# Optimization experiments

Hardware: AMD Instinct MI355X
Metric: run time of the kernel (lower is better)

The kernel has to match this reference:

```python
import jax, jax.numpy as jnp
import numpy as np

B, N, K, C, CE, H = 2, 2048, 48, 128, 128, 128
IN = 2 * C + CE  # 384
AGG_SCALE = 30.0
LN_EPS = 1e-5


def setup_inputs() -> dict:
    key = jax.random.key(0)
    ks = jax.random.split(key, 12)
    inp = {
        "node_h": jax.random.normal(ks[0], (B, N, C), jnp.float32),
        "edge_h": jax.random.normal(ks[1], (B, N, K, CE), jnp.float32),
        "edge_index": jax.random.randint(ks[2], (B, N, K), 0, N, jnp.int64),
        # message MLP: Linear(IN,H) GELU Linear(H,H) GELU Linear(H,C)
        "W1": jax.random.normal(ks[3], (IN, H), jnp.float32) / np.sqrt(IN),
        "b1": jnp.zeros((H,), jnp.float32),
        "W2": jax.random.normal(ks[4], (H, H), jnp.float32) / np.sqrt(H),
        "b2": jnp.zeros((H,), jnp.float32),
        "W3": jax.random.normal(ks[5], (H, C), jnp.float32) / np.sqrt(H),
        "b3": jnp.zeros((C,), jnp.float32),
        "Wu": jax.random.normal(ks[6], (C, C), jnp.float32) / np.sqrt(C),
        "bu": jnp.zeros((C,), jnp.float32),
        "ln_g": jnp.ones((C,), jnp.float32),
        "ln_b": jnp.zeros((C,), jnp.float32),
    }
    return inp


def _layer_norm(x, g, b):
    mu = jnp.mean(x, axis=-1, keepdims=True)
    var = jnp.var(x, axis=-1, keepdims=True)
    return (x - mu) * jax.lax.rsqrt(var + LN_EPS) * g + b


def _gelu(x):
    return jax.nn.gelu(x, approximate=False)  # torch nn.GELU default (erf)


def reference(node_h, edge_h, edge_index, W1, b1, W2, b2, W3, b3, Wu, bu, ln_g, ln_b):
    b, n, k = edge_index.shape
    c = node_h.shape[-1]
    # gather neighbor node features: (B,N,K,C)
    node_j = jnp.take_along_axis(
        node_h, edge_index.reshape(b, n * k)[..., None], axis=1
    ).reshape(b, n, k, c)
    node_i = jnp.broadcast_to(node_h[:, :, None, :], (b, n, k, c))
    edge_packed = jnp.concatenate([node_i, node_j, edge_h], axis=-1)  # (B,N,K,IN)
    # message MLP
    h = _gelu(edge_packed @ W1 + b1)
    h = _gelu(h @ W2 + b2)
    messages = (h @ W3 + b3).sum(axis=-2) / AGG_SCALE  # (B,N,C)
    # dropout is identity in eval mode
    updated_nodes = _layer_norm(node_h + messages, ln_g, ln_b)
    node_updates = updated_nodes @ Wu + bu
    out = _layer_norm(node_h + node_updates, ln_g, ln_b)
    return out
```

## Files before the change

kernel.cpp:

```cpp
#include <hip/hip_runtime.h>
#include <hip/hip_bf16.h>
#include <math.h>

#define Bn   2
#define Nn   2048
#define Kn   48
#define Cn   128
#define G2   16

typedef short bf16x8 __attribute__((ext_vector_type(8)));
typedef float f32x4  __attribute__((ext_vector_type(4)));

#if __has_builtin(__builtin_amdgcn_cvt_pk_bf16_f32)
#define HAS_PK 1
#endif

__device__ __forceinline__ short f2bf(float f) {
  union { float f; unsigned u; } v; v.f = f;
  unsigned r = v.u + 0x7fffu + ((v.u >> 16) & 1u);
  return (short)(r >> 16);
}

__device__ __forceinline__ unsigned pk2(float a, float b) {
#ifdef HAS_PK
  auto p = __builtin_amdgcn_cvt_pk_bf16_f32(a, b);
  return __builtin_bit_cast(unsigned, p);
#else
  return (unsigned)(unsigned short)f2bf(a) | ((unsigned)(unsigned short)f2bf(b) << 16);
#endif
}

__device__ __forceinline__ float gelu_f(float x) {
  float z = x * (-2.3021991f - 0.10294200f * x * x);
  float e = __builtin_amdgcn_exp2f(z);
  return x * __builtin_amdgcn_rcpf(1.0f + e);
}

__global__ void pack_weights(const float* __restrict__ W1,
                             const float* __restrict__ W2,
                             const float* __restrict__ W3,
                             const float* __restrict__ Wu,
                             short* __restrict__ ws) {
  int tid = blockIdx.x * blockDim.x + threadIdx.x;
  if (tid >= 192 * 64) return;
  int lane = tid & 63;
  int tile = tid >> 6;
  const float* W; short* dst;
  if (tile < 32)       { W = W1;         dst = ws; }
  else if (tile < 96)  { W = W1 + 16384; dst = ws + 16384; tile -= 32; }
  else if (tile < 128) { W = W2;         dst = ws + 49152; tile -= 96; }
  else if (tile < 160) { W = W3;         dst = ws + 65536; tile -= 128; }
  else                 { W = Wu;         dst = ws + 81920; tile -= 160; }
  int kt = tile >> 3, nt = tile & 7;
  int n  = nt * 16 + (lane & 15);
  int k0 = kt * 32 + (lane >> 4) * 8;
  union { short s[8]; bf16x8 v; } u8;
#pragma unroll
  for (int j = 0; j < 8; j++) u8.s[j] = f2bf(W[(k0 + j) * 128 + n]);
  *reinterpret_cast<bf16x8*>(dst + (tile << 9) + lane * 8) = u8.v;
}

__global__ __launch_bounds__(512, 6)
void node_update_kernel(const float* __restrict__ node_h,
                        const float* __restrict__ edge_h,
                        const int*   __restrict__ edge_index,
                        const short* __restrict__ wpack,
                        const float* __restrict__ b1,
                        const float* __restrict__ b2,
                        float* __restrict__ hs_out) {
  __shared__ __align__(16) char smem[50048];
  short* Xs    = (short*)smem;
  short* H1s   = (short*)(smem + 24576);
  short* nhb   = (short*)(smem + 49152);
  int*   idx_s = (int*)  (smem + 49664);

  const int tid  = threadIdx.x;
  const int n0   = blockIdx.x * 2;
  const int bb   = n0 >> 11;
  const int lane = tid & 63;
  const int wave = tid >> 6;
  const int lr   = lane & 15;
  const int lq   = lane >> 4;

  const short* W1i = wpack;
  const short* W1e = wpack + 16384;
  const short* W2p = wpack + 49152;

  if (tid < 256) {
    nhb[tid] = f2bf(node_h[(size_t)n0 * Cn + tid]);
  } else if (tid < 352) {
    idx_s[tid - 256] = edge_index[n0 * Kn + (tid - 256)];
  }
  __syncthreads();

  {
    const int w  = tid & 31;
    const int rr = tid >> 5;
#pragma unroll
    for (int k = 0; k < 6; k++) {
      int r = rr + k * 16;
      const float* src = (w < 16)
          ? node_h + (size_t)(bb * Nn + idx_s[r]) * Cn + w * 8
          : edge_h + ((size_t)n0 * Kn + r) * Cn + (w - 16) * 8;
      float4 v0 = *reinterpret_cast<const float4*>(src);
      float4 v1 = *reinterpret_cast<const float4*>(src + 4);
      uint4 p;
      p.x = pk2(v0.x, v0.y); p.y = pk2(v0.z, v0.w);
      p.z = pk2(v1.x, v1.y); p.w = pk2(v1.z, v1.w);
      *reinterpret_cast<uint4*>(&Xs[r * 256 + ((w ^ (r & 7)) << 3)]) = p;
    }
  }

  f32x4 accY[2] = {};
#pragma unroll
  for (int kt = 0; kt < 4; kt++) {
    bf16x8 avA = {}, avB = {};
    if (lr == 0) {
      avA = *reinterpret_cast<const bf16x8*>(&nhb[kt * 32 + lq * 8]);
      avB = *reinterpret_cast<const bf16x8*>(&nhb[128 + kt * 32 + lq * 8]);
    }
    bf16x8 bv = *reinterpret_cast<const bf16x8*>(W1i + ((kt * 8 + wave) << 9) + lane * 8);
    accY[0] = __builtin_amdgcn_mfma_f32_16x16x32_bf16(avA, bv, accY[0], 0, 0, 0);
    accY[1] = __builtin_amdgcn_mfma_f32_16x16x32_bf16(avB, bv, accY[1], 0, 0, 0);
  }
  __syncthreads();

  f32x4 acc[6] = {};
#pragma unroll
  for (int kt = 0; kt < 8; kt++) {
    bf16x8 bf = *reinterpret_cast<const bf16x8*>(W1e + ((kt * 8 + wave) << 9) + lane * 8);
    int sw = (((kt * 4 + lq) ^ (lr & 7)) << 3);
#pragma unroll
    for (int m = 0; m < 6; m++) {
      bf16x8 a = *reinterpret_cast<const bf16x8*>(&Xs[(m * 16 + lr) * 256 + sw]);
      acc[m] = __builtin_amdgcn_mfma_f32_16x16x32_bf16(a, bf, acc[m], 0, 0, 0);
    }
  }
  __syncthreads();

  {
    int col = wave * 16 + lr;
    float yiA = __shfl(accY[0][0], lr) + b1[col];
    float yiB = __shfl(accY[1][0], lr) + b1[col];
    int g = col >> 3, cl = col & 7;
#pragma unroll
    for (int mt = 0; mt < 6; mt++) {
      float yi = (mt < 3) ? yiA : yiB;
      int r0 = mt * 16 + lq * 4;
      float g0 = gelu_f(acc[mt][0] + yi);
      float g1 = gelu_f(acc[mt][1] + yi);
      float g2 = gelu_f(acc[mt][2] + yi);
      float g3 = gelu_f(acc[mt][3] + yi);
      unsigned p01 = pk2(g0, g1), p23 = pk2(g2, g3);
      H1s[(r0 + 0) * 128 + ((g ^ ((r0 + 0) & 7)) << 3) + cl] = (short)(p01 & 0xffff);
      H1s[(r0 + 1) * 128 + ((g ^ ((r0 + 1) & 7)) << 3) + cl] = (short)(p01 >> 16);
      H1s[(r0 + 2) * 128 + ((g ^ ((r0 + 2) & 7)) << 3) + cl] = (short)(p23 & 0xffff);
      H1s[(r0 + 3) * 128 + ((g ^ ((r0 + 3) & 7)) << 3) + cl] = (short)(p23 >> 16);
    }
  }
  __syncthreads();

  f32x4 acc2[6] = {};
#pragma unroll
  for (int kt = 0; kt < 4; kt++) {
    bf16x8 bf = *reinterpret_cast<const bf16x8*>(W2p + ((kt * 8 + wave) << 9) + lane * 8);
    int sw = (((kt * 4 + lq) ^ (lr & 7)) << 3);
#pragma unroll
    for (int m = 0; m < 6; m++) {
      bf16x8 a = *reinterpret_cast<const bf16x8*>(&H1s[(m * 16 + lr) * 128 + sw]);
      acc2[m] = __builtin_amdgcn_mfma_f32_16x16x32_bf16(a, bf, acc2[m], 0, 0, 0);
    }
  }
  {
    int col = wave * 16 + lr;
    float bias = b2[col];
    float sA = 0.f, sB = 0.f;
#pragma unroll
    for (int mt = 0; mt < 3; mt++)
#pragma unroll
      for (int r = 0; r < 4; r++) {
        sA += gelu_f(acc2[mt][r] + bias);
        sB += gelu_f(acc2[mt + 3][r] + bias);
      }
    sA += __shfl_xor(sA, 16);
    sA += __shfl_xor(sA, 32);
    sB += __shfl_xor(sB, 16);
    sB += __shfl_xor(sB, 32);
    if (lq == 0) {
      hs_out[(size_t)n0 * Cn + col]       = sA;
      hs_out[(size_t)(n0 + 1) * Cn + col] = sB;
    }
  }
}

__global__ __launch_bounds__(256, 4)
void tail_kernel(const float* __restrict__ node_h,
                 const short* __restrict__ wpack,
                 const float* __restrict__ b3,
                 const float* __restrict__ bu,
                 const float* __restrict__ ln_g,
                 const float* __restrict__ ln_b,
                 float* __restrict__ out) {
  __shared__ __align__(16) char sm2[24832];
  short* hsB = (short*)sm2;
  float* nhr = (float*)(sm2 + 4096);
  float* xs  = (float*)(sm2 + 12288);
  short* usB = (short*)(sm2 + 20736);

  const int tid  = threadIdx.x;
  const int lane = tid & 63;
  const int wave = tid >> 6;
  const int lr   = lane & 15;
  const int lq   = lane >> 4;
  const int n0   = blockIdx.x * G2;

  const short* W3p = wpack + 65536;
  const short* Wup = wpack + 81920;

  {
    int row = tid >> 4, seg = tid & 15;
    const float* p = node_h + (size_t)(n0 + row) * Cn + seg * 8;
    float4 a0 = *reinterpret_cast<const float4*>(p);
    float4 a1 = *reinterpret_cast<const float4*>(p + 4);
    *reinterpret_cast<float4*>(&nhr[row * 128 + seg * 8])     = a0;
    *reinterpret_cast<float4*>(&nhr[row * 128 + seg * 8 + 4]) = a1;
    const float* q = out + (size_t)(n0 + row) * Cn + seg * 8;
    float4 c0 = *reinterpret_cast<const float4*>(q);
    float4 c1 = *reinterpret_cast<const float4*>(q + 4);
    uint4 pk;
    pk.x = pk2(c0.x, c0.y); pk.y = pk2(c0.z, c0.w);
    pk.z = pk2(c1.x, c1.y); pk.w = pk2(c1.z, c1.w);
    *reinterpret_cast<uint4*>(&hsB[row * 128 + ((seg ^ (row & 7)) << 3)]) = pk;
  }
  __syncthreads();

  f32x4 am[2] = {};
#pragma unroll
  for (int kt = 0; kt < 4; kt++) {
    bf16x8 av = *reinterpret_cast<const bf16x8*>(&hsB[lr * 128 + (((kt * 4 + lq) ^ (lr & 7)) << 3)]);
    bf16x8 bv0 = *reinterpret_cast<const bf16x8*>(W3p + ((kt * 8 + wave * 2 + 0) << 9) + lane * 8);
    bf16x8 bv1 = *reinterpret_cast<const bf16x8*>(W3p + ((kt * 8 + wave * 2 + 1) << 9) + lane * 8);
    am[0] = __builtin_amdgcn_mfma_f32_16x16x32_bf16(av, bv0, am[0], 0, 0, 0);
    am[1] = __builtin_amdgcn_mfma_f32_16x16x32_bf16(av, bv1, am[1], 0, 0, 0);
  }
#pragma unroll
  for (int j = 0; j < 2; j++) {
    int col = (wave * 2 + j) * 16 + lr;
    float bb = 48.0f * b3[col];
#pragma unroll
    for (int r = 0; r < 4; r++) {
      int row = lq * 4 + r;
      xs[row * 132 + col] = nhr[row * 128 + col] + (am[j][r] + bb) * (1.0f / 30.0f);
    }
  }
  __syncthreads();

  const float lg1 = ln_g[lane],      lb1v = ln_b[lane];
  const float lg2 = ln_g[lane + 64], lb2v = ln_b[lane + 64];
#pragma unroll
  for (int s = 0; s < 4; s++) {
    int row = wave * 4 + s;
    float v1 = xs[row * 132 + lane];
    float v2 = xs[row * 132 + lane + 64];
    float s1 = v1 + v2, s2 = v1 * v1 + v2 * v2;
#pragma unroll
    for (int off = 32; off >= 1; off >>= 1) {
      s1 += __shfl_xor(s1, off);
      s2 += __shfl_xor(s2, off);
    }
    float mu = s1 * (1.f / 128.f);
    float var = s2 * (1.f / 128.f) - mu * mu;
    float rstd = rsqrtf(var + 1e-5f);
    unsigned u12 = pk2((v1 - mu) * rstd * lg1 + lb1v,
                       (v2 - mu) * rstd * lg2 + lb2v);
    int sw = (row & 7);
    usB[row * 128 + (((lane >> 3) ^ sw) << 3) + (lane & 7)]       = (short)(u12 & 0xffff);
    usB[row * 128 + ((((lane >> 3) + 8) ^ sw) << 3) + (lane & 7)] = (short)(u12 >> 16);
  }
  __syncthreads();

  f32x4 au[2] = {};
#pragma unroll
  for (int kt = 0; kt < 4; kt++) {
    bf16x8 av = *reinterpret_cast<const bf16x8*>(&usB[lr * 128 + (((kt * 4 + lq) ^ (lr & 7)) << 3)]);
    bf16x8 bv0 = *reinterpret_cast<const bf16x8*>(Wup + ((kt * 8 + wave * 2 + 0) << 9) + lane * 8);
    bf16x8 bv1 = *reinterpret_cast<const bf16x8*>(Wup + ((kt * 8 + wave * 2 + 1) << 9) + lane * 8);
    au[0] = __builtin_amdgcn_mfma_f32_16x16x32_bf16(av, bv0, au[0], 0, 0, 0);
    au[1] = __builtin_amdgcn_mfma_f32_16x16x32_bf16(av, bv1, au[1], 0, 0, 0);
  }
  __syncthreads();
#pragma unroll
  for (int j = 0; j < 2; j++) {
    int col = (wave * 2 + j) * 16 + lr;
    float bb = bu[col];
#pragma unroll
    for (int r = 0; r < 4; r++) {
      int row = lq * 4 + r;
      xs[row * 132 + col] = nhr[row * 128 + col] + au[j][r] + bb;
    }
  }
  __syncthreads();

#pragma unroll
  for (int s = 0; s < 4; s++) {
    int row = wave * 4 + s;
    float v1 = xs[row * 132 + lane];
    float v2 = xs[row * 132 + lane + 64];
    float s1 = v1 + v2, s2 = v1 * v1 + v2 * v2;
#pragma unroll
    for (int off = 32; off >= 1; off >>= 1) {
      s1 += __shfl_xor(s1, off);
      s2 += __shfl_xor(s2, off);
    }
    float mu = s1 * (1.f / 128.f);
    float var = s2 * (1.f / 128.f) - mu * mu;
    float rstd = rsqrtf(var + 1e-5f);
    out[(size_t)(n0 + row) * Cn + lane]      = (v1 - mu) * rstd * lg1 + lb1v;
    out[(size_t)(n0 + row) * Cn + lane + 64] = (v2 - mu) * rstd * lg2 + lb2v;
  }
}

extern "C" void kernel_launch(void* const* d_in, const int* in_sizes, int n_in,
                              void* d_out, int out_size, void* d_ws, size_t ws_size,
                              hipStream_t stream) {
  const float* node_h     = (const float*)d_in[0];
  const float* edge_h     = (const float*)d_in[1];
  const int*   edge_index = (const int*)  d_in[2];
  const float* W1 = (const float*)d_in[3];
  const float* b1 = (const float*)d_in[4];
  const float* W2 = (const float*)d_in[5];
  const float* b2 = (const float*)d_in[6];
  const float* W3 = (const float*)d_in[7];
  const float* b3 = (const float*)d_in[8];
  const float* Wu = (const float*)d_in[9];
  const float* bu = (const float*)d_in[10];
  const float* ln_g = (const float*)d_in[11];
  const float* ln_b = (const float*)d_in[12];
  float* out   = (float*)d_out;
  short* wpack = (short*)d_ws;

  pack_weights<<<48, 256, 0, stream>>>(W1, W2, W3, Wu, wpack);
  node_update_kernel<<<(Bn * Nn) / 2, 512, 0, stream>>>(
      node_h, edge_h, edge_index, wpack, b1, b2, out);
  tail_kernel<<<(Bn * Nn) / G2, 256, 0, stream>>>(
      node_h, wpack, b3, bu, ln_g, ln_b, out);
}
```

Baseline: 206.7 us.

## Prefetch weights into registers and overlap gather loads with node-projection MFMA

After: 282.2 us. 1.37x slower.

```diff
diff --git a/kernel.cpp b/kernel.cpp
--- a/kernel.cpp
+++ b/kernel.cpp
@@ -86,6 +86,20 @@
   const short* W1e = wpack + 16384;
   const short* W2p = wpack + 49152;
 
+  bf16x8 w1i[4], w1e[8], w2f[4];
+#pragma unroll
+  for (int kt = 0; kt < 4; kt++)
+    w1i[kt] = *reinterpret_cast<const bf16x8*>(W1i + ((kt * 8 + wave) << 9) + lane * 8);
+#pragma unroll
+  for (int kt = 0; kt < 8; kt++)
+    w1e[kt] = *reinterpret_cast<const bf16x8*>(W1e + ((kt * 8 + wave) << 9) + lane * 8);
+#pragma unroll
+  for (int kt = 0; kt < 4; kt++)
+    w2f[kt] = *reinterpret_cast<const bf16x8*>(W2p + ((kt * 8 + wave) << 9) + lane * 8);
+  const int colw = wave * 16 + lr;
+  const float b1v = b1[colw];
+  const float b2v = b2[colw];
+
   if (tid < 256) {
     nhb[tid] = f2bf(node_h[(size_t)n0 * Cn + tid]);
   } else if (tid < 352) {
@@ -93,25 +107,21 @@
   }
   __syncthreads();
 
-  {
-    const int w  = tid & 31;
-    const int rr = tid >> 5;
-#pragma unroll
-    for (int k = 0; k < 6; k++) {
-      int r = rr + k * 16;
-      const float* src = (w < 16)
-          ? node_h + (size_t)(bb * Nn + idx_s[r]) * Cn + w * 8
-          : edge_h + ((size_t)n0 * Kn + r) * Cn + (w - 16) * 8;
-      float4 v0 = *reinterpret_cast<const float4*>(src);
-      float4 v1 = *reinterpret_cast<const float4*>(src + 4);
-      uint4 p;
-      p.x = pk2(v0.x, v0.y); p.y = pk2(v0.z, v0.w);
-      p.z = pk2(v1.x, v1.y); p.w = pk2(v1.z, v1.w);
-      *reinterpret_cast<uint4*>(&Xs[r * 256 + ((w ^ (r & 7)) << 3)]) = p;
-    }
+  const int w  = tid & 31;
+  const int rr = tid >> 5;
+  float4 v0[6], v1[6];
+#pragma unroll
+  for (int k = 0; k < 6; k++) {
+    int r = rr + k * 16;
+    const float* src = (w < 16)
+        ? node_h + (size_t)(bb * Nn + idx_s[r]) * Cn + w * 8
+        : edge_h + ((size_t)n0 * Kn + r) * Cn + (w - 16) * 8;
+    v0[k] = *reinterpret_cast<const float4*>(src);
+    v1[k] = *reinterpret_cast<const float4*>(src + 4);
   }
 
   f32x4 accY[2] = {};
+  __builtin_amdgcn_s_setprio(1);
 #pragma unroll
   for (int kt = 0; kt < 4; kt++) {
     bf16x8 avA = {}, avB = {};
@@ -119,30 +129,39 @@
       avA = *reinterpret_cast<const bf16x8*>(&nhb[kt * 32 + lq * 8]);
       avB = *reinterpret_cast<const bf16x8*>(&nhb[128 + kt * 32 + lq * 8]);
     }
-    bf16x8 bv = *reinterpret_cast<const bf16x8*>(W1i + ((kt * 8 + wave) << 9) + lane * 8);
-    accY[0] = __builtin_amdgcn_mfma_f32_16x16x32_bf16(avA, bv, accY[0], 0, 0, 0);
-    accY[1] = __builtin_amdgcn_mfma_f32_16x16x32_bf16(avB, bv, accY[1], 0, 0, 0);
+    accY[0] = __builtin_amdgcn_mfma_f32_16x16x32_bf16(avA, w1i[kt], accY[0], 0, 0, 0);
+    accY[1] = __builtin_amdgcn_mfma_f32_16x16x32_bf16(avB, w1i[kt], accY[1], 0, 0, 0);
+  }
+  __builtin_amdgcn_s_setprio(0);
+
+#pragma unroll
+  for (int k = 0; k < 6; k++) {
+    int r = rr + k * 16;
+    uint4 p;
+    p.x = pk2(v0[k].x, v0[k].y); p.y = pk2(v0[k].z, v0[k].w);
+    p.z = pk2(v1[k].x, v1[k].y); p.w = pk2(v1[k].z, v1[k].w);
+    *reinterpret_cast<uint4*>(&Xs[r * 256 + ((w ^ (r & 7)) << 3)]) = p;
   }
   __syncthreads();
 
   f32x4 acc[6] = {};
+  __builtin_amdgcn_s_setprio(1);
 #pragma unroll
   for (int kt = 0; kt < 8; kt++) {
-    bf16x8 bf = *reinterpret_cast<const bf16x8*>(W1e + ((kt * 8 + wave) << 9) + lane * 8);
     int sw = (((kt * 4 + lq) ^ (lr & 7)) << 3);
 #pragma unroll
     for (int m = 0; m < 6; m++) {
       bf16x8 a = *reinterpret_cast<const bf16x8*>(&Xs[(m * 16 + lr) * 256 + sw]);
-      acc[m] = __builtin_amdgcn_mfma_f32_16x16x32_bf16(a, bf, acc[m], 0, 0, 0);
-    }
-  }
+      acc[m] = __builtin_amdgcn_mfma_f32_16x16x32_bf16(a, w1e[kt], acc[m], 0, 0, 0);
+    }
+  }
+  __builtin_amdgcn_s_setprio(0);
   __syncthreads();
 
   {
-    int col = wave * 16 + lr;
-    float yiA = __shfl(accY[0][0], lr) + b1[col];
-    float yiB = __shfl(accY[1][0], lr) + b1[col];
-    int g = col >> 3, cl = col & 7;
+    float yiA = __shfl(accY[0][0], lr) + b1v;
+    float yiB = __shfl(accY[1][0], lr) + b1v;
+    int g = colw >> 3, cl = colw & 7;
 #pragma unroll
     for (int mt = 0; mt < 6; mt++) {
       float yi = (mt < 3) ? yiA : yiB;
@@ -161,34 +180,33 @@
   __syncthreads();
 
   f32x4 acc2[6] = {};
-#pragma unroll
-  for (int kt = 0; kt < 4; kt++) {
-    bf16x8 bf = *reinterpret_cast<const bf16x8*>(W2p + ((kt * 8 + wave) << 9) + lane * 8);
+  __builtin_amdgcn_s_setprio(1);
+#pragma unroll
+  for (int kt = 0; kt < 4; kt++) {
     int sw = (((kt * 4 + lq) ^ (lr & 7)) << 3);
 #pragma unroll
     for (int m = 0; m < 6; m++) {
       bf16x8 a = *reinterpret_cast<const bf16x8*>(&H1s[(m * 16 + lr) * 128 + sw]);
-      acc2[m] = __builtin_amdgcn_mfma_f32_16x16x32_bf16(a, bf, acc2[m], 0, 0, 0);
-    }
-  }
+      acc2[m] = __builtin_amdgcn_mfma_f32_16x16x32_bf16(a, w2f[kt], acc2[m], 0, 0, 0);
+    }
+  }
+  __builtin_amdgcn_s_setprio(0);
   {
-    int col = wave * 16 + lr;
-    float bias = b2[col];
     float sA = 0.f, sB = 0.f;
 #pragma unroll
     for (int mt = 0; mt < 3; mt++)
 #pragma unroll
       for (int r = 0; r < 4; r++) {
-        sA += gelu_f(acc2[mt][r] + bias);
-        sB += gelu_f(acc2[mt + 3][r] + bias);
+        sA += gelu_f(acc2[mt][r] + b2v);
+        sB += gelu_f(acc2[mt + 3][r] + b2v);
       }
     sA += __shfl_xor(sA, 16);
     sA += __shfl_xor(sA, 32);
     sB += __shfl_xor(sB, 16);
     sB += __shfl_xor(sB, 32);
     if (lq == 0) {
-      hs_out[(size_t)n0 * Cn + col]       = sA;
-      hs_out[(size_t)(n0 + 1) * Cn + col] = sB;
+      hs_out[(size_t)n0 * Cn + colw]       = sA;
+      hs_out[(size_t)(n0 + 1) * Cn + colw] = sB;
     }
   }
 }
@@ -216,6 +234,15 @@
 
   const short* W3p = wpack + 65536;
   const short* Wup = wpack + 81920;
+
+  bf16x8 w3f[8], wuf[8];
+#pragma unroll
+  for (int kt = 0; kt < 4; kt++) {
+    w3f[2 * kt + 0] = *reinterpret_cast<const bf16x8*>(W3p + ((kt * 8 + wave * 2 + 0) << 9) + lane * 8);
+    w3f[2 * kt + 1] = *reinterpret_cast<const bf16x8*>(W3p + ((kt * 8 + wave * 2 + 1) << 9) + lane * 8);
+    wuf[2 * kt + 0] = *reinterpret_cast<const bf16x8*>(Wup + ((kt * 8 + wave * 2 + 0) << 9) + lane * 8);
+    wuf[2 * kt + 1] = *reinterpret_cast<const bf16x8*>(Wup + ((kt * 8 + wave * 2 + 1) << 9) + lane * 8);
+  }
 
   {
     int row = tid >> 4, seg = tid & 15;
@@ -238,10 +265,8 @@
 #pragma unroll
   for (int kt = 0; kt < 4; kt++) {
     bf16x8 av = *reinterpret_cast<const bf16x8*>(&hsB[lr * 128 + (((kt * 4 + lq) ^ (lr & 7)) << 3)]);
-    bf16x8 bv0 = *reinterpret_cast<const bf16x8*>(W3p + ((kt * 8 + wave * 2 + 0) << 9) + lane * 8);
-    bf16x8 bv1 = *reinterpret_cast<const bf16x8*>(W3p + ((kt * 8 + wave * 2 + 1) << 9) + lane * 8);
-    am[0] = __builtin_amdgcn_mfma_f32_16x16x32_bf16(av, bv0, am[0], 0, 0, 0);
-    am[1] = __builtin_amdgcn_mfma_f32_16x16x32_bf16(av, bv1, am[1], 0, 0, 0);
+    am[0] = __builtin_amdgcn_mfma_f32_16x16x32_bf16(av, w3f[2 * kt + 0], am[0], 0, 0, 0);
+    am[1] = __builtin_amdgcn_mfma_f32_16x16x32_bf16(av, w3f[2 * kt + 1], am[1], 0, 0, 0);
   }
 #pragma unroll
   for (int j = 0; j < 2; j++) {
@@ -283,10 +308,8 @@
 #pragma unroll
   for (int kt = 0; kt < 4; kt++) {
     bf16x8 av = *reinterpret_cast<const bf16x8*>(&usB[lr * 128 + (((kt * 4 + lq) ^ (lr & 7)) << 3)]);
-    bf16x8 bv0 = *reinterpret_cast<const bf16x8*>(Wup + ((kt * 8 + wave * 2 + 0) << 9) + lane * 8);
-    bf16x8 bv1 = *reinterpret_cast<const bf16x8*>(Wup + ((kt * 8 + wave * 2 + 1) << 9) + lane * 8);
-    au[0] = __builtin_amdgcn_mfma_f32_16x16x32_bf16(av, bv0, au[0], 0, 0, 0);
-    au[1] = __builtin_amdgcn_mfma_f32_16x16x32_bf16(av, bv1, au[1], 0, 0, 0);
+    au[0] = __builtin_amdgcn_mfma_f32_16x16x32_bf16(av, wuf[2 * kt + 0], au[0], 0, 0, 0);
+    au[1] = __builtin_amdgcn_mfma_f32_16x16x32_bf16(av, wuf[2 * kt + 1], au[1], 0, 0, 0);
   }
   __syncthreads();
 #pragma unroll
```

## Split X staging into two K-halves to halve shared memory and raise occupancy

Applied to the files above, without the earlier changes.

Result: no change. 209.0 us (+1.1%).

```diff
diff --git a/kernel.cpp b/kernel.cpp
--- a/kernel.cpp
+++ b/kernel.cpp
@@ -60,7 +60,7 @@
   *reinterpret_cast<bf16x8*>(dst + (tile << 9) + lane * 8) = u8.v;
 }
 
-__global__ __launch_bounds__(512, 6)
+__global__ __launch_bounds__(512, 8)
 void node_update_kernel(const float* __restrict__ node_h,
                         const float* __restrict__ edge_h,
                         const int*   __restrict__ edge_index,
@@ -68,11 +68,11 @@
                         const float* __restrict__ b1,
                         const float* __restrict__ b2,
                         float* __restrict__ hs_out) {
-  __shared__ __align__(16) char smem[50048];
+  __shared__ __align__(16) char smem[25472];
   short* Xs    = (short*)smem;
-  short* H1s   = (short*)(smem + 24576);
-  short* nhb   = (short*)(smem + 49152);
-  int*   idx_s = (int*)  (smem + 49664);
+  short* H1s   = (short*)smem;
+  short* nhb   = (short*)(smem + 24576);
+  int*   idx_s = (int*)  (smem + 25088);
 
   const int tid  = threadIdx.x;
   const int n0   = blockIdx.x * 2;
@@ -93,23 +93,20 @@
   }
   __syncthreads();
 
-  {
-    const int w  = tid & 31;
-    const int rr = tid >> 5;
-#pragma unroll
-    for (int k = 0; k < 6; k++) {
-      int r = rr + k * 16;
-      const float* src = (w < 16)
-          ? node_h + (size_t)(bb * Nn + idx_s[r]) * Cn + w * 8
-          : edge_h + ((size_t)n0 * Kn + r) * Cn + (w - 16) * 8;
-      float4 v0 = *reinterpret_cast<const float4*>(src);
-      float4 v1 = *reinterpret_cast<const float4*>(src + 4);
-      uint4 p;
-      p.x = pk2(v0.x, v0.y); p.y = pk2(v0.z, v0.w);
-      p.z = pk2(v1.x, v1.y); p.w = pk2(v1.z, v1.w);
-      *reinterpret_cast<uint4*>(&Xs[r * 256 + ((w ^ (r & 7)) << 3)]) = p;
-    }
-  }
+  const int gw = tid & 15;
+  const int gr = tid >> 4;
+#pragma unroll
+  for (int k = 0; k < 3; k++) {
+    int r = gr + k * 32;
+    const float* src = node_h + (size_t)(bb * Nn + idx_s[r]) * Cn + gw * 8;
+    float4 v0 = *reinterpret_cast<const float4*>(src);
+    float4 v1 = *reinterpret_cast<const float4*>(src + 4);
+    uint4 p;
+    p.x = pk2(v0.x, v0.y); p.y = pk2(v0.z, v0.w);
+    p.z = pk2(v1.x, v1.y); p.w = pk2(v1.z, v1.w);
+    *reinterpret_cast<uint4*>(&Xs[r * 128 + ((gw ^ (r & 7)) << 3)]) = p;
+  }
+  __syncthreads();
 
   f32x4 accY[2] = {};
 #pragma unroll
@@ -123,16 +120,40 @@
     accY[0] = __builtin_amdgcn_mfma_f32_16x16x32_bf16(avA, bv, accY[0], 0, 0, 0);
     accY[1] = __builtin_amdgcn_mfma_f32_16x16x32_bf16(avB, bv, accY[1], 0, 0, 0);
   }
-  __syncthreads();
 
   f32x4 acc[6] = {};
 #pragma unroll
-  for (int kt = 0; kt < 8; kt++) {
+  for (int kt = 0; kt < 4; kt++) {
     bf16x8 bf = *reinterpret_cast<const bf16x8*>(W1e + ((kt * 8 + wave) << 9) + lane * 8);
     int sw = (((kt * 4 + lq) ^ (lr & 7)) << 3);
 #pragma unroll
     for (int m = 0; m < 6; m++) {
-      bf16x8 a = *reinterpret_cast<const bf16x8*>(&Xs[(m * 16 + lr) * 256 + sw]);
+      bf16x8 a = *reinterpret_cast<const bf16x8*>(&Xs[(m * 16 + lr) * 128 + sw]);
+      acc[m] = __builtin_amdgcn_mfma_f32_16x16x32_bf16(a, bf, acc[m], 0, 0, 0);
+    }
+  }
+  __syncthreads();
+
+#pragma unroll
+  for (int k = 0; k < 3; k++) {
+    int r = gr + k * 32;
+    const float* src = edge_h + ((size_t)n0 * Kn + r) * Cn + gw * 8;
+    float4 v0 = *reinterpret_cast<const float4*>(src);
+    float4 v1 = *reinterpret_cast<const float4*>(src + 4);
+    uint4 p;
+    p.x = pk2(v0.x, v0.y); p.y = pk2(v0.z, v0.w);
+    p.z = pk2(v1.x, v1.y); p.w = pk2(v1.z, v1.w);
+    *reinterpret_cast<uint4*>(&Xs[r * 128 + ((gw ^ (r & 7)) << 3)]) = p;
+  }
+  __syncthreads();
+
+#pragma unroll
+  for (int kt = 4; kt < 8; kt++) {
+    bf16x8 bf = *reinterpret_cast<const bf16x8*>(W1e + ((kt * 8 + wave) << 9) + lane * 8);
+    int sw = ((((kt - 4) * 4 + lq) ^ (lr & 7)) << 3);
+#pragma unroll
+    for (int m = 0; m < 6; m++) {
+      bf16x8 a = *reinterpret_cast<const bf16x8*>(&Xs[(m * 16 + lr) * 128 + sw]);
       acc[m] = __builtin_amdgcn_mfma_f32_16x16x32_bf16(a, bf, acc[m], 0, 0, 0);
     }
   }
```
